# Kernel tuning notes

Measured on AMD Instinct MI355X. Metric: run time of the kernel, lower is better.

Reference implementation:

```python
import jax, jax.numpy as jnp
import numpy as np

DIM = 768
HID = 3072
HID2 = HID // 2
MAX_LEVEL = 8
N_LEV = MAX_LEVEL + 1
BATCH, SEQ = 2, 2048
EPS = 1e-5


def _layernorm(x, gamma, beta):
    m = jnp.mean(x, axis=-1, keepdims=True)
    v = jnp.mean(jnp.square(x - m), axis=-1, keepdims=True)
    return (x - m) * jax.lax.rsqrt(v + EPS) * gamma + beta


def setup_inputs() -> dict:
    key = jax.random.key(0)
    ks = jax.random.split(key, 12)
    s = 0.02
    return {
        "x": jax.random.normal(ks[0], (BATCH, SEQ, DIM), dtype=jnp.float32),
        "levels_info": jax.random.randint(ks[1], (SEQ, 4), 0, N_LEV, dtype=jnp.int32),
        "gamma": jnp.ones((DIM,), dtype=jnp.float32),
        "beta": jnp.zeros((DIM,), dtype=jnp.float32),
        "W1": jax.random.normal(ks[2], (DIM, HID), dtype=jnp.float32) * s,
        "b1": jnp.zeros((HID,), dtype=jnp.float32),
        "W2": jax.random.normal(ks[3], (HID, DIM), dtype=jnp.float32) * s,
        "b2": jnp.zeros((DIM,), dtype=jnp.float32),
        "A1": jax.random.normal(ks[4], (N_LEV, DIM, HID2), dtype=jnp.float32) * s,
        "a1b": jnp.zeros((N_LEV, HID2), dtype=jnp.float32),
        "A2": jax.random.normal(ks[5], (N_LEV, HID2, DIM), dtype=jnp.float32) * s,
        "a2b": jnp.zeros((N_LEV, DIM), dtype=jnp.float32),
        "lmw": jnp.ones((N_LEV,), dtype=jnp.float32)
        + jax.random.normal(ks[6], (N_LEV,), dtype=jnp.float32) * 0.1,
    }


def reference(x, levels_info, gamma, beta, W1, b1, W2, b2, A1, a1b, A2, a2b, lmw):
    # x: [B,S,D]
    x_norm = _layernorm(x, gamma, beta)
    # main MLP: Linear -> GELU (exact, torch default) -> Linear; dropout=0 is identity
    h = jax.nn.gelu(jnp.einsum("bsd,dh->bsh", x_norm, W1) + b1, approximate=False)
    main_out = jnp.einsum("bsh,hd->bsd", h, W2) + b2

    # per-token depth-indexed adapter routing
    depths = jnp.clip(levels_info[:, 0], 0, MAX_LEVEL)  # [S]
    level_adapted = jnp.zeros_like(main_out)
    for lvl in range(N_LEV):  # small fixed expert set
        mask = (depths == lvl).astype(x.dtype)[None, :, None]  # [1,S,1]
        hl = jax.nn.relu(jnp.einsum("bsd,dh->bsh", x_norm, A1[lvl]) + a1b[lvl])
        level_adapted = level_adapted + mask * (
            jnp.einsum("bsh,hd->bsd", hl, A2[lvl]) + a2b[lvl]
        )

    # softmax over the sequence axis (faithful to F.softmax(..., dim=0))
    mix = jax.nn.softmax(lmw[depths], axis=0)[None, :, None]  # [1,S,1]
    return main_out * (1.0 - mix) + level_adapted * mix
```

## Files before the change

### kernel.cpp

```cpp
#include <hip/hip_runtime.h>
#include <hip/hip_bf16.h>
#include <math.h>

typedef __bf16 bf16;
typedef __bf16 bf16x4 __attribute__((ext_vector_type(4)));
typedef __bf16 bf16x8 __attribute__((ext_vector_type(8)));
typedef float f32x4 __attribute__((ext_vector_type(4)));

#define DIM 768
#define HID 3072
#define HID2 1536
#define NLEV 9
#define SEQ 2048
#define ROWS 4096
#define MAXPAD 5248
#define MAXTILES 41

__device__ __forceinline__ void gld16(const void* g, void* l) {
    __builtin_amdgcn_global_load_lds(
        (const __attribute__((address_space(1))) void*)g,
        (__attribute__((address_space(3))) void*)l, 16, 0, 0);
}

__device__ __forceinline__ float fast_gelu(float v) {
    float v2 = v * v;
    float twou = v * (1.59576912f + 0.071354816f * v2);
    float t = __expf(twou);
    return v * t / (t + 1.0f);
}


__device__ __forceinline__ void ln_body(int row, float* sm,
                                        const float* __restrict__ x,
                                        const float* __restrict__ gamma,
                                        const float* __restrict__ beta,
                                        bf16* __restrict__ xn) {
    int tid = threadIdx.x;
    const float* xr = x + (size_t)row * DIM;
    float v0 = xr[tid], v1 = xr[tid + 256], v2 = xr[tid + 512];
    float s = v0 + v1 + v2;
    float q = v0 * v0 + v1 * v1 + v2 * v2;
    for (int off = 32; off; off >>= 1) {
        s += __shfl_down(s, off, 64);
        q += __shfl_down(q, off, 64);
    }
    int wv = tid >> 6, ln = tid & 63;
    if (ln == 0) { sm[wv] = s; sm[4 + wv] = q; }
    __syncthreads();
    if (tid == 0) {
        float S = sm[0] + sm[1] + sm[2] + sm[3];
        float Q = sm[4] + sm[5] + sm[6] + sm[7];
        float m = S * (1.0f / DIM);
        float var = Q * (1.0f / DIM) - m * m;
        sm[8] = m;
        sm[9] = rsqrtf(var + 1e-5f);
    }
    __syncthreads();
    float m = sm[8], r = sm[9];
    bf16* xo = xn + (size_t)row * DIM;
    xo[tid]       = (bf16)((v0 - m) * r * gamma[tid]       + beta[tid]);
    xo[tid + 256] = (bf16)((v1 - m) * r * gamma[tid + 256] + beta[tid + 256]);
    xo[tid + 512] = (bf16)((v2 - m) * r * gamma[tid + 512] + beta[tid + 512]);
}

__device__ __forceinline__ void transpose_body64(float* sm,
                                                 const float* __restrict__ inb,
                                                 bf16* __restrict__ outb,
                                                 int R, int C, int bx, int by) {
    int tid = threadIdx.x;
    int ty = tid >> 4;
    int tx4 = (tid & 15) * 4;
#pragma unroll
    for (int p = 0; p < 4; p++) {
        int rloc = p * 16 + ty;
        int row = by * 64 + rloc;
        float4 v = *(const float4*)(inb + (size_t)row * C + bx * 64 + tx4);
        sm[rloc * 65 + tx4 + 0] = v.x;
        sm[rloc * 65 + tx4 + 1] = v.y;
        sm[rloc * 65 + tx4 + 2] = v.z;
        sm[rloc * 65 + tx4 + 3] = v.w;
    }
    __syncthreads();
    int ch = tid & 7;
    int ocb = tid >> 3;
#pragma unroll
    for (int p = 0; p < 2; p++) {
        int oc = p * 32 + ocb;
        bf16x8 tmp;
#pragma unroll
        for (int k = 0; k < 8; k++) tmp[k] = (bf16)sm[(ch * 8 + k) * 65 + oc];
        *(bf16x8*)(outb + (size_t)(bx * 64 + oc) * R + by * 64 + ch * 8) = tmp;
    }
}

__device__ __forceinline__ void routing_body(float* sm,
                                             const int* __restrict__ levels_info,
                                             const float* __restrict__ lmw,
                                             float* __restrict__ mix,
                                             int* __restrict__ row_index,
                                             int* __restrict__ tile_meta,
                                             float* __restrict__ zbuf) {
    int* cnt = (int*)sm;
    int* cur = cnt + NLEV;
    int* off = cur + NLEV;
    float* mixv = (float*)(off + NLEV);
    int tid = threadIdx.x;
    if (tid < NLEV) { cnt[tid] = 0; cur[tid] = 0; }
    __syncthreads();
    for (int s = tid; s < SEQ; s += 256) {
        int d = levels_info[s * 4];
        d = d < 0 ? 0 : (d > 8 ? 8 : d);
        atomicAdd(&cnt[d], 1);
    }
    for (int i = tid; i < MAXPAD; i += 256) row_index[i] = -1;
    if (tid < 16) zbuf[tid] = 0.0f;
    __syncthreads();
    if (tid == 0) {
        float mx = lmw[0];
        for (int l = 1; l < NLEV; l++) mx = fmaxf(mx, lmw[l]);
        float denom = 0.f;
        for (int l = 0; l < NLEV; l++) denom += (float)cnt[l] * expf(lmw[l] - mx);
        float inv = 1.0f / denom;
        int running = 0, t = 0;
        for (int l = 0; l < NLEV; l++) {
            mixv[l] = expf(lmw[l] - mx) * inv;
            off[l] = running;
            int seg = (2 * cnt[l] + 127) & ~127;
            for (int k = 0; k < seg / 128; k++) tile_meta[t++] = l;
            running += seg;
        }
        for (; t < MAXTILES; t++) tile_meta[t] = -1;
    }
    __syncthreads();
    for (int s = tid; s < SEQ; s += 256) {
        int d = levels_info[s * 4];
        d = d < 0 ? 0 : (d > 8 ? 8 : d);
        int p = atomicAdd(&cur[d], 2);
        row_index[off[d] + p]     = s;
        row_index[off[d] + p + 1] = s + SEQ;
        mix[s] = mixv[d];
    }
}

__global__ __launch_bounds__(256) void prep_kernel(const float* __restrict__ x,
                                                   const int* __restrict__ levels_info,
                                                   const float* __restrict__ gamma,
                                                   const float* __restrict__ beta,
                                                   const float* __restrict__ W1,
                                                   const float* __restrict__ W2,
                                                   const float* __restrict__ A1,
                                                   const float* __restrict__ A2,
                                                   const float* __restrict__ lmw,
                                                   bf16* __restrict__ Xn,
                                                   bf16* __restrict__ W1t,
                                                   bf16* __restrict__ W2t,
                                                   bf16* __restrict__ A1t,
                                                   bf16* __restrict__ A2t,
                                                   float* __restrict__ mix,
                                                   int* __restrict__ row_index,
                                                   int* __restrict__ tile_meta,
                                                   float* __restrict__ zbuf) {
    __shared__ __align__(16) float sm[64 * 65];
    int bid = blockIdx.x;
    if (bid == 0) { routing_body(sm, levels_info, lmw, mix, row_index, tile_meta, zbuf); return; }
    bid -= 1;
    if (bid < ROWS) { ln_body(bid, sm, x, gamma, beta, Xn); return; }
    bid -= ROWS;
    if (bid < 576) {
        transpose_body64(sm, W1, W1t, DIM, HID, bid % 48, bid / 48);
        return;
    }
    bid -= 576;
    if (bid < 576) {
        transpose_body64(sm, W2, W2t, HID, DIM, bid % 12, bid / 12);
        return;
    }
    bid -= 576;
    if (bid < 2592) {
        int bz = bid / 288, r = bid % 288;
        transpose_body64(sm, A1 + (size_t)bz * DIM * HID2, A1t + (size_t)bz * DIM * HID2,
                         DIM, HID2, r % 24, r / 24);
        return;
    }
    bid -= 2592;
    {
        int bz = bid / 288, r = bid % 288;
        transpose_body64(sm, A2 + (size_t)bz * HID2 * DIM, A2t + (size_t)bz * HID2 * DIM,
                         HID2, DIM, r % 12, r / 12);
    }
}

__device__ __forceinline__ void gemm_loop_db(const bf16* ga0, const bf16* ga1,
                                             int stepa0, int stepa1,
                                             const bf16* gb0, const bf16* gb1, int stepb,
                                             bf16* As, bf16* Bs,
                                             f32x4 (&acc)[4][4], int ktiles) {
    int tid = threadIdx.x;
    int wv = tid >> 6;
    int lane = tid & 63;
    int wm = wv >> 1, wn = wv & 1;
    int swz = (lane >> 1) & 3;
    int achunk = ((lane >> 4) ^ swz) * 8;
    int aoff = ((wm * 64) + (lane & 15)) * 32 + achunk;
    int boff = ((wn * 64) + (lane & 15)) * 32 + achunk;
    gld16(ga0, As + wv * 512);
    gld16(ga1, As + 2048 + wv * 512);
    gld16(gb0, Bs + wv * 512);
    gld16(gb1, Bs + 2048 + wv * 512);
    ga0 += stepa0; ga1 += stepa1; gb0 += stepb; gb1 += stepb;
    for (int kt = 0; kt < ktiles; ++kt) {
        __syncthreads();
        int cur = (kt & 1) << 12;
        int nxt = cur ^ 4096;
        if (kt + 1 < ktiles) {
            gld16(ga0, As + nxt + wv * 512);
            gld16(ga1, As + nxt + 2048 + wv * 512);
            gld16(gb0, Bs + nxt + wv * 512);
            gld16(gb1, Bs + nxt + 2048 + wv * 512);
            ga0 += stepa0; ga1 += stepa1; gb0 += stepb; gb1 += stepb;
        }
        bf16x8 af[4], bfr[4];
#pragma unroll
        for (int i = 0; i < 4; i++) af[i] = *(const bf16x8*)(As + cur + aoff + i * 512);
#pragma unroll
        for (int j = 0; j < 4; j++) bfr[j] = *(const bf16x8*)(Bs + cur + boff + j * 512);
#pragma unroll
        for (int i = 0; i < 4; i++)
#pragma unroll
            for (int j = 0; j < 4; j++)
                acc[i][j] = __builtin_amdgcn_mfma_f32_16x16x32_bf16(af[i], bfr[j], acc[i][j], 0, 0, 0);
    }
}

#define ACC_INIT(acc) \
    _Pragma("unroll") for (int i = 0; i < 4; i++) \
    _Pragma("unroll") for (int j = 0; j < 4; j++) acc[i][j] = (f32x4){0.f, 0.f, 0.f, 0.f};

#define SWZ_CG(tid) (((tid) & 3) ^ (((tid) >> 3) & 3))

__global__ __launch_bounds__(256) void mlp1_kernel(const bf16* __restrict__ Xn,
                                                   const bf16* __restrict__ W1t,
                                                   const float* __restrict__ b1,
                                                   bf16* __restrict__ H,
                                                   const bf16* __restrict__ A1t,
                                                   const float* __restrict__ a1b,
                                                   const int* __restrict__ row_index,
                                                   const int* __restrict__ tile_meta,
                                                   const bf16* __restrict__ zbuf,
                                                   bf16* __restrict__ HL) {
    __shared__ __align__(16) bf16 As[8192], Bs[8192];
    int bid = blockIdx.x, tid = threadIdx.x;
    int r0 = tid >> 2, cg = SWZ_CG(tid);
    int lane = tid & 63, wv = tid >> 6, wm = wv >> 1, wn = wv & 1;
    f32x4 acc[4][4];
    ACC_INIT(acc);

    if (bid < 768) {
        int mb = (bid & 7) + 8 * ((bid >> 3) & 3);
        int nb = bid >> 5;
        const bf16* ga0 = Xn + (size_t)(mb * 128 + r0) * DIM + cg * 8;
        const bf16* ga1 = ga0 + (size_t)64 * DIM;
        const bf16* gb0 = W1t + (size_t)(nb * 128 + r0) * DIM + cg * 8;
        const bf16* gb1 = gb0 + (size_t)64 * DIM;
        gemm_loop_db(ga0, ga1, 32, 32, gb0, gb1, 32, As, Bs, acc, DIM / 32);
        int rbase = mb * 128 + wm * 64 + ((lane >> 4) << 2);
        int cbase = nb * 128 + wn * 64 + (lane & 15);
#pragma unroll
        for (int j = 0; j < 4; j++) {
            int c = cbase + j * 16;
            float bias = b1[c];
#pragma unroll
            for (int i = 0; i < 4; i++)
#pragma unroll
                for (int r = 0; r < 4; r++) {
                    int row = rbase + i * 16 + r;
                    float v = acc[i][j][r] + bias;
                    H[(size_t)row * HID + c] = (bf16)fast_gelu(v);
                }
        }
    } else {
        int t2 = bid - 768;
        int t = t2 % MAXTILES, nb = t2 / MAXTILES;
        int lvl = tile_meta[t];
        if (lvl < 0) return;
        int ridx0 = row_index[t * 128 + r0];
        int ridx1 = row_index[t * 128 + 64 + r0];
        const bf16* ga0 = (ridx0 >= 0) ? (Xn + (size_t)ridx0 * DIM + cg * 8) : zbuf;
        const bf16* ga1 = (ridx1 >= 0) ? (Xn + (size_t)ridx1 * DIM + cg * 8) : zbuf;
        int sa0 = (ridx0 >= 0) ? 32 : 0;
        int sa1 = (ridx1 >= 0) ? 32 : 0;
        const bf16* Bl = A1t + (size_t)lvl * HID2 * DIM;
        const bf16* gb0 = Bl + (size_t)(nb * 128 + r0) * DIM + cg * 8;
        const bf16* gb1 = gb0 + (size_t)64 * DIM;
        gemm_loop_db(ga0, ga1, sa0, sa1, gb0, gb1, 32, As, Bs, acc, DIM / 32);
        int rbase = wm * 64 + ((lane >> 4) << 2);
        int cbase = nb * 128 + wn * 64 + (lane & 15);
#pragma unroll
        for (int j = 0; j < 4; j++) {
            int c = cbase + j * 16;
            float bias = a1b[lvl * HID2 + c];
#pragma unroll
            for (int i = 0; i < 4; i++)
#pragma unroll
                for (int r = 0; r < 4; r++) {
                    int rl = rbase + i * 16 + r;
                    float v = acc[i][j][r] + bias;
                    HL[(size_t)(t * 128 + rl) * HID2 + c] = (bf16)fmaxf(v, 0.0f);
                }
        }
    }
}

__global__ __launch_bounds__(256) void mlp2_kernel(const bf16* __restrict__ H,
                                                   const bf16* __restrict__ W2t,
                                                   bf16* __restrict__ part,
                                                   const bf16* __restrict__ HL,
                                                   const bf16* __restrict__ A2t,
                                                   const float* __restrict__ a2b,
                                                   const int* __restrict__ row_index,
                                                   const int* __restrict__ tile_meta,
                                                   bf16* __restrict__ apart) {
    __shared__ __align__(16) bf16 As[8192], Bs[8192];
    int bid = blockIdx.x, tid = threadIdx.x;
    int r0 = tid >> 2, cg = SWZ_CG(tid);
    int lane = tid & 63, wv = tid >> 6, wm = wv >> 1, wn = wv & 1;
    f32x4 acc[4][4];
    ACC_INIT(acc);

    if (bid < 768) {
        int mb = (bid & 7) + 8 * ((bid >> 3) & 3);
        int rest = bid >> 5;
        int nb = rest % 6;
        int ks = rest / 6;
        const bf16* ga0 = H + (size_t)(mb * 128 + r0) * HID + ks * 768 + cg * 8;
        const bf16* ga1 = ga0 + (size_t)64 * HID;
        const bf16* gb0 = W2t + (size_t)(nb * 128 + r0) * HID + ks * 768 + cg * 8;
        const bf16* gb1 = gb0 + (size_t)64 * HID;
        gemm_loop_db(ga0, ga1, 32, 32, gb0, gb1, 32, As, Bs, acc, 24);
        bf16* pk = part + (size_t)ks * ROWS * DIM;
        int rbase = mb * 128 + wm * 64 + ((lane >> 4) << 2);
        int cbase = nb * 128 + wn * 64 + (lane & 15);
#pragma unroll
        for (int j = 0; j < 4; j++) {
            int c = cbase + j * 16;
#pragma unroll
            for (int i = 0; i < 4; i++)
#pragma unroll
                for (int r = 0; r < 4; r++) {
                    int row = rbase + i * 16 + r;
                    pk[(size_t)row * DIM + c] = (bf16)acc[i][j][r];
                }
        }
    } else {
        int t2 = bid - 768;
        int t = t2 % MAXTILES;
        int rest = t2 / MAXTILES;
        int nb = rest % 6;
        int ks = rest / 6;
        int lvl = tile_meta[t];
        if (lvl < 0) return;
        const bf16* ga0 = HL + (size_t)(t * 128 + r0) * HID2 + ks * 768 + cg * 8;
        const bf16* ga1 = ga0 + (size_t)64 * HID2;
        const bf16* Bl = A2t + (size_t)lvl * DIM * HID2;
        const bf16* gb0 = Bl + (size_t)(nb * 128 + r0) * HID2 + ks * 768 + cg * 8;
        const bf16* gb1 = gb0 + (size_t)64 * HID2;
        gemm_loop_db(ga0, ga1, 32, 32, gb0, gb1, 32, As, Bs, acc, 24);
        bf16* apk = apart + (size_t)ks * ROWS * DIM;
        int rbase = wm * 64 + ((lane >> 4) << 2);
        int cbase = nb * 128 + wn * 64 + (lane & 15);
#pragma unroll
        for (int i = 0; i < 4; i++)
#pragma unroll
            for (int r = 0; r < 4; r++) {
                int rl = rbase + i * 16 + r;
                int rg = row_index[t * 128 + rl];
                if (rg >= 0) {
#pragma unroll
                    for (int j = 0; j < 4; j++) {
                        int c = cbase + j * 16;
                        float v = acc[i][j][r] + (ks == 0 ? a2b[lvl * DIM + c] : 0.0f);
                        apk[(size_t)rg * DIM + c] = (bf16)v;
                    }
                }
            }
    }
}

__global__ __launch_bounds__(256) void combine_kernel(const bf16* __restrict__ part,
                                                      const bf16* __restrict__ apart,
                                                      const float* __restrict__ b2,
                                                      const float* __restrict__ mix,
                                                      float* __restrict__ out) {
    int i = blockIdx.x * 256 + threadIdx.x;
    int base = i * 4;
    int row = base / DIM;
    int c = base - row * DIM;
    float mx = mix[row & (SEQ - 1)];
    bf16x4 p0 = *(const bf16x4*)(part + base);
    bf16x4 p1 = *(const bf16x4*)(part + (size_t)1 * ROWS * DIM + base);
    bf16x4 p2 = *(const bf16x4*)(part + (size_t)2 * ROWS * DIM + base);
    bf16x4 p3 = *(const bf16x4*)(part + (size_t)3 * ROWS * DIM + base);
    bf16x4 a0 = *(const bf16x4*)(apart + base);
    bf16x4 a1 = *(const bf16x4*)(apart + (size_t)1 * ROWS * DIM + base);
    float4 o;
    float* po = &o.x;
#pragma unroll
    for (int k = 0; k < 4; k++) {
        float main_v = (float)p0[k] + (float)p1[k] + (float)p2[k] + (float)p3[k] + b2[c + k];
        float ap_v = (float)a0[k] + (float)a1[k];
        po[k] = (1.0f - mx) * main_v + mx * ap_v;
    }
    *(float4*)(out + base) = o;
}

extern "C" void kernel_launch(void* const* d_in, const int* in_sizes, int n_in,
                              void* d_out, int out_size, void* d_ws, size_t ws_size,
                              hipStream_t stream) {
    const float* x    = (const float*)d_in[0];
    const int* levels = (const int*)d_in[1];
    const float* gamma= (const float*)d_in[2];
    const float* beta = (const float*)d_in[3];
    const float* W1   = (const float*)d_in[4];
    const float* b1   = (const float*)d_in[5];
    const float* W2   = (const float*)d_in[6];
    const float* b2   = (const float*)d_in[7];
    const float* A1   = (const float*)d_in[8];
    const float* a1b  = (const float*)d_in[9];
    const float* A2   = (const float*)d_in[10];
    const float* a2b  = (const float*)d_in[11];
    const float* lmw  = (const float*)d_in[12];
    float* out = (float*)d_out;

    char* p = (char*)d_ws;
    auto alloc = [&](size_t bytes) {
        char* r = p;
        p += (bytes + 255) & ~(size_t)255;
        return r;
    };
    bf16* Xn   = (bf16*)alloc((size_t)ROWS * DIM * 2);
    bf16* W1t  = (bf16*)alloc((size_t)HID * DIM * 2);
    bf16* W2t  = (bf16*)alloc((size_t)DIM * HID * 2);
    bf16* A1t  = (bf16*)alloc((size_t)NLEV * HID2 * DIM * 2);
    bf16* A2t  = (bf16*)alloc((size_t)NLEV * DIM * HID2 * 2);
    bf16* H    = (bf16*)alloc((size_t)ROWS * HID * 2);
    bf16* HL   = (bf16*)alloc((size_t)MAXPAD * HID2 * 2);
    bf16* part = (bf16*)alloc((size_t)4 * ROWS * DIM * 2);
    bf16* apart= (bf16*)alloc((size_t)2 * ROWS * DIM * 2);
    float* mix = (float*)alloc(SEQ * 4);
    int* row_index = (int*)alloc(MAXPAD * 4);
    int* tile_meta = (int*)alloc(MAXTILES * 4);
    float* zbuf    = (float*)alloc(64);

    prep_kernel<<<dim3(1 + ROWS + 576 + 576 + 2592 + 2592), dim3(256), 0, stream>>>(
        x, levels, gamma, beta, W1, W2, A1, A2, lmw,
        Xn, W1t, W2t, A1t, A2t, mix, row_index, tile_meta, zbuf);

    mlp1_kernel<<<dim3(768 + MAXTILES * 12), dim3(256), 0, stream>>>(
        Xn, W1t, b1, H, A1t, a1b, row_index, tile_meta, (const bf16*)zbuf, HL);

    mlp2_kernel<<<dim3(768 + MAXTILES * 12), dim3(256), 0, stream>>>(
        H, W2t, part, HL, A2t, a2b, row_index, tile_meta, apart);

    combine_kernel<<<dim3(ROWS * DIM / 1024), dim3(256), 0, stream>>>(
        part, apart, b2, mix, out);
}
```

Measured before the change: 299.7 us.

## Replace LDS-staged GEMM loop with direct global-to-register MFMA operand loads

```diff
diff --git a/kernel.cpp b/kernel.cpp
--- a/kernel.cpp
+++ b/kernel.cpp
@@ -15,12 +15,6 @@
 #define ROWS 4096
 #define MAXPAD 5248
 #define MAXTILES 41
-
-__device__ __forceinline__ void gld16(const void* g, void* l) {
-    __builtin_amdgcn_global_load_lds(
-        (const __attribute__((address_space(1))) void*)g,
-        (__attribute__((address_space(3))) void*)l, 16, 0, 0);
-}
 
 __device__ __forceinline__ float fast_gelu(float v) {
     float v2 = v * v;
@@ -113,7 +107,7 @@
         atomicAdd(&cnt[d], 1);
     }
     for (int i = tid; i < MAXPAD; i += 256) row_index[i] = -1;
-    if (tid < 16) zbuf[tid] = 0.0f;
+    for (int i = tid; i < 512; i += 256) zbuf[i] = 0.0f;
     __syncthreads();
     if (tid == 0) {
         float mx = lmw[0];
@@ -190,53 +184,42 @@
     }
 }
 
-__device__ __forceinline__ void gemm_loop_db(const bf16* ga0, const bf16* ga1,
-                                             int stepa0, int stepa1,
-                                             const bf16* gb0, const bf16* gb1, int stepb,
-                                             bf16* As, bf16* Bs,
-                                             f32x4 (&acc)[4][4], int ktiles) {
-    int tid = threadIdx.x;
-    int wv = tid >> 6;
-    int lane = tid & 63;
-    int wm = wv >> 1, wn = wv & 1;
-    int swz = (lane >> 1) & 3;
-    int achunk = ((lane >> 4) ^ swz) * 8;
-    int aoff = ((wm * 64) + (lane & 15)) * 32 + achunk;
-    int boff = ((wn * 64) + (lane & 15)) * 32 + achunk;
-    gld16(ga0, As + wv * 512);
-    gld16(ga1, As + 2048 + wv * 512);
-    gld16(gb0, Bs + wv * 512);
-    gld16(gb1, Bs + 2048 + wv * 512);
-    ga0 += stepa0; ga1 += stepa1; gb0 += stepb; gb1 += stepb;
-    for (int kt = 0; kt < ktiles; ++kt) {
-        __syncthreads();
-        int cur = (kt & 1) << 12;
-        int nxt = cur ^ 4096;
-        if (kt + 1 < ktiles) {
-            gld16(ga0, As + nxt + wv * 512);
-            gld16(ga1, As + nxt + 2048 + wv * 512);
-            gld16(gb0, Bs + nxt + wv * 512);
-            gld16(gb1, Bs + nxt + 2048 + wv * 512);
-            ga0 += stepa0; ga1 += stepa1; gb0 += stepb; gb1 += stepb;
-        }
-        bf16x8 af[4], bfr[4];
-#pragma unroll
-        for (int i = 0; i < 4; i++) af[i] = *(const bf16x8*)(As + cur + aoff + i * 512);
-#pragma unroll
-        for (int j = 0; j < 4; j++) bfr[j] = *(const bf16x8*)(Bs + cur + boff + j * 512);
+__device__ __forceinline__ void gemm_k768(const bf16* pa0, const bf16* pa1,
+                                          const bf16* pa2, const bf16* pa3,
+                                          const bf16* pb0, const bf16* pb1,
+                                          const bf16* pb2, const bf16* pb3,
+                                          f32x4 (&acc)[4][4]) {
+    const bf16* pa[4] = {pa0, pa1, pa2, pa3};
+    const bf16* pb[4] = {pb0, pb1, pb2, pb3};
+    bf16x8 af[2][4], bfr[2][4];
+#pragma unroll
+    for (int i = 0; i < 4; i++) {
+        af[0][i]  = *(const bf16x8*)(pa[i]);
+        bfr[0][i] = *(const bf16x8*)(pb[i]);
+        af[1][i]  = *(const bf16x8*)(pa[i] + 32);
+        bfr[1][i] = *(const bf16x8*)(pb[i] + 32);
+    }
+#pragma unroll
+    for (int kt = 0; kt < 24; kt++) {
+        int s = kt & 1;
 #pragma unroll
         for (int i = 0; i < 4; i++)
 #pragma unroll
             for (int j = 0; j < 4; j++)
-                acc[i][j] = __builtin_amdgcn_mfma_f32_16x16x32_bf16(af[i], bfr[j], acc[i][j], 0, 0, 0);
+                acc[i][j] = __builtin_amdgcn_mfma_f32_16x16x32_bf16(af[s][i], bfr[s][j], acc[i][j], 0, 0, 0);
+        if (kt + 2 < 24) {
+#pragma unroll
+            for (int i = 0; i < 4; i++) {
+                af[s][i]  = *(const bf16x8*)(pa[i] + (kt + 2) * 32);
+                bfr[s][i] = *(const bf16x8*)(pb[i] + (kt + 2) * 32);
+            }
+        }
     }
 }
 
 #define ACC_INIT(acc) \
     _Pragma("unroll") for (int i = 0; i < 4; i++) \
     _Pragma("unroll") for (int j = 0; j < 4; j++) acc[i][j] = (f32x4){0.f, 0.f, 0.f, 0.f};
-
-#define SWZ_CG(tid) (((tid) & 3) ^ (((tid) >> 3) & 3))
 
 __global__ __launch_bounds__(256) void mlp1_kernel(const bf16* __restrict__ Xn,
                                                    const bf16* __restrict__ W1t,
@@ -248,23 +231,25 @@
                                                    const int* __restrict__ tile_meta,
                                                    const bf16* __restrict__ zbuf,
                                                    bf16* __restrict__ HL) {
-    __shared__ __align__(16) bf16 As[8192], Bs[8192];
     int bid = blockIdx.x, tid = threadIdx.x;
-    int r0 = tid >> 2, cg = SWZ_CG(tid);
     int lane = tid & 63, wv = tid >> 6, wm = wv >> 1, wn = wv & 1;
+    int lr = lane & 15, lc = (lane >> 4) * 8;
     f32x4 acc[4][4];
     ACC_INIT(acc);
 
     if (bid < 768) {
-        int mb = (bid & 7) + 8 * ((bid >> 3) & 3);
-        int nb = bid >> 5;
-        const bf16* ga0 = Xn + (size_t)(mb * 128 + r0) * DIM + cg * 8;
-        const bf16* ga1 = ga0 + (size_t)64 * DIM;
-        const bf16* gb0 = W1t + (size_t)(nb * 128 + r0) * DIM + cg * 8;
-        const bf16* gb1 = gb0 + (size_t)64 * DIM;
-        gemm_loop_db(ga0, ga1, 32, 32, gb0, gb1, 32, As, Bs, acc, DIM / 32);
+        int nb = (bid & 7) * 3 + ((bid >> 3) % 3);
+        int mb = bid / 24;
+        const bf16* pa[4];
+        const bf16* pb[4];
+#pragma unroll
+        for (int i = 0; i < 4; i++) {
+            pa[i] = Xn  + (size_t)(mb * 128 + wm * 64 + i * 16 + lr) * DIM + lc;
+            pb[i] = W1t + (size_t)(nb * 128 + wn * 64 + i * 16 + lr) * DIM + lc;
+        }
+        gemm_k768(pa[0], pa[1], pa[2], pa[3], pb[0], pb[1], pb[2], pb[3], acc);
         int rbase = mb * 128 + wm * 64 + ((lane >> 4) << 2);
-        int cbase = nb * 128 + wn * 64 + (lane & 15);
+        int cbase = nb * 128 + wn * 64 + lr;
 #pragma unroll
         for (int j = 0; j < 4; j++) {
             int c = cbase + j * 16;
@@ -274,27 +259,26 @@
 #pragma unroll
                 for (int r = 0; r < 4; r++) {
                     int row = rbase + i * 16 + r;
-                    float v = acc[i][j][r] + bias;
-                    H[(size_t)row * HID + c] = (bf16)fast_gelu(v);
+                    H[(size_t)row * HID + c] = (bf16)fast_gelu(acc[i][j][r] + bias);
                 }
         }
     } else {
         int t2 = bid - 768;
-        int t = t2 % MAXTILES, nb = t2 / MAXTILES;
+        int nb = t2 % 12, t = t2 / 12;
         int lvl = tile_meta[t];
         if (lvl < 0) return;
-        int ridx0 = row_index[t * 128 + r0];
-        int ridx1 = row_index[t * 128 + 64 + r0];
-        const bf16* ga0 = (ridx0 >= 0) ? (Xn + (size_t)ridx0 * DIM + cg * 8) : zbuf;
-        const bf16* ga1 = (ridx1 >= 0) ? (Xn + (size_t)ridx1 * DIM + cg * 8) : zbuf;
-        int sa0 = (ridx0 >= 0) ? 32 : 0;
-        int sa1 = (ridx1 >= 0) ? 32 : 0;
+        const bf16* pa[4];
+        const bf16* pb[4];
         const bf16* Bl = A1t + (size_t)lvl * HID2 * DIM;
-        const bf16* gb0 = Bl + (size_t)(nb * 128 + r0) * DIM + cg * 8;
-        const bf16* gb1 = gb0 + (size_t)64 * DIM;
-        gemm_loop_db(ga0, ga1, sa0, sa1, gb0, gb1, 32, As, Bs, acc, DIM / 32);
+#pragma unroll
+        for (int i = 0; i < 4; i++) {
+            int ridx = row_index[t * 128 + wm * 64 + i * 16 + lr];
+            pa[i] = (ridx >= 0) ? (Xn + (size_t)ridx * DIM + lc) : (zbuf + lc);
+            pb[i] = Bl + (size_t)(nb * 128 + wn * 64 + i * 16 + lr) * DIM + lc;
+        }
+        gemm_k768(pa[0], pa[1], pa[2], pa[3], pb[0], pb[1], pb[2], pb[3], acc);
         int rbase = wm * 64 + ((lane >> 4) << 2);
-        int cbase = nb * 128 + wn * 64 + (lane & 15);
+        int cbase = nb * 128 + wn * 64 + lr;
 #pragma unroll
         for (int j = 0; j < 4; j++) {
             int c = cbase + j * 16;
@@ -304,8 +288,7 @@
 #pragma unroll
                 for (int r = 0; r < 4; r++) {
                     int rl = rbase + i * 16 + r;
-                    float v = acc[i][j][r] + bias;
-                    HL[(size_t)(t * 128 + rl) * HID2 + c] = (bf16)fmaxf(v, 0.0f);
+                    HL[(size_t)(t * 128 + rl) * HID2 + c] = (bf16)fmaxf(acc[i][j][r] + bias, 0.0f);
                 }
         }
     }
@@ -320,26 +303,27 @@
                                                    const int* __restrict__ row_index,
                                                    const int* __restrict__ tile_meta,
                                                    bf16* __restrict__ apart) {
-    __shared__ __align__(16) bf16 As[8192], Bs[8192];
     int bid = blockIdx.x, tid = threadIdx.x;
-    int r0 = tid >> 2, cg = SWZ_CG(tid);
     int lane = tid & 63, wv = tid >> 6, wm = wv >> 1, wn = wv & 1;
+    int lr = lane & 15, lc = (lane >> 4) * 8;
     f32x4 acc[4][4];
     ACC_INIT(acc);
 
     if (bid < 768) {
-        int mb = (bid & 7) + 8 * ((bid >> 3) & 3);
-        int rest = bid >> 5;
-        int nb = rest % 6;
-        int ks = rest / 6;
-        const bf16* ga0 = H + (size_t)(mb * 128 + r0) * HID + ks * 768 + cg * 8;
-        const bf16* ga1 = ga0 + (size_t)64 * HID;
-        const bf16* gb0 = W2t + (size_t)(nb * 128 + r0) * HID + ks * 768 + cg * 8;
-        const bf16* gb1 = gb0 + (size_t)64 * HID;
-        gemm_loop_db(ga0, ga1, 32, 32, gb0, gb1, 32, As, Bs, acc, 24);
+        int c24 = (bid & 7) * 3 + ((bid >> 3) % 3);
+        int nb = c24 >> 2, ks = c24 & 3;
+        int mb = bid / 24;
+        const bf16* pa[4];
+        const bf16* pb[4];
+#pragma unroll
+        for (int i = 0; i < 4; i++) {
+            pa[i] = H   + (size_t)(mb * 128 + wm * 64 + i * 16 + lr) * HID + ks * 768 + lc;
+            pb[i] = W2t + (size_t)(nb * 128 + wn * 64 + i * 16 + lr) * HID + ks * 768 + lc;
+        }
+        gemm_k768(pa[0], pa[1], pa[2], pa[3], pb[0], pb[1], pb[2], pb[3], acc);
         bf16* pk = part + (size_t)ks * ROWS * DIM;
         int rbase = mb * 128 + wm * 64 + ((lane >> 4) << 2);
-        int cbase = nb * 128 + wn * 64 + (lane & 15);
+        int cbase = nb * 128 + wn * 64 + lr;
 #pragma unroll
         for (int j = 0; j < 4; j++) {
             int c = cbase + j * 16;
@@ -353,21 +337,23 @@
         }
     } else {
         int t2 = bid - 768;
-        int t = t2 % MAXTILES;
-        int rest = t2 / MAXTILES;
-        int nb = rest % 6;
-        int ks = rest / 6;
+        int cc = t2 % 12;
+        int nb = cc >> 1, ks = cc & 1;
+        int t = t2 / 12;
         int lvl = tile_meta[t];
         if (lvl < 0) return;
-        const bf16* ga0 = HL + (size_t)(t * 128 + r0) * HID2 + ks * 768 + cg * 8;
-        const bf16* ga1 = ga0 + (size_t)64 * HID2;
+        const bf16* pa[4];
+        const bf16* pb[4];
         const bf16* Bl = A2t + (size_t)lvl * DIM * HID2;
-        const bf16* gb0 = Bl + (size_t)(nb * 128 + r0) * HID2 + ks * 768 + cg * 8;
-        const bf16* gb1 = gb0 + (size_t)64 * HID2;
-        gemm_loop_db(ga0, ga1, 32, 32, gb0, gb1, 32, As, Bs, acc, 24);
+#pragma unroll
+        for (int i = 0; i < 4; i++) {
+            pa[i] = HL + (size_t)(t * 128 + wm * 64 + i * 16 + lr) * HID2 + ks * 768 + lc;
+            pb[i] = Bl + (size_t)(nb * 128 + wn * 64 + i * 16 + lr) * HID2 + ks * 768 + lc;
+        }
+        gemm_k768(pa[0], pa[1], pa[2], pa[3], pb[0], pb[1], pb[2], pb[3], acc);
         bf16* apk = apart + (size_t)ks * ROWS * DIM;
         int rbase = wm * 64 + ((lane >> 4) << 2);
-        int cbase = nb * 128 + wn * 64 + (lane & 15);
+        int cbase = nb * 128 + wn * 64 + lr;
 #pragma unroll
         for (int i = 0; i < 4; i++)
 #pragma unroll
@@ -449,7 +435,7 @@
     float* mix = (float*)alloc(SEQ * 4);
     int* row_index = (int*)alloc(MAXPAD * 4);
     int* tile_meta = (int*)alloc(MAXTILES * 4);
-    float* zbuf    = (float*)alloc(64);
+    float* zbuf    = (float*)alloc(2048);
 
     prep_kernel<<<dim3(1 + ROWS + 576 + 576 + 2592 + 2592), dim3(256), 0, stream>>>(
         x, levels, gamma, beta, W1, W2, A1, A2, lmw,
```

Measured after the change: 409.1 us. +36.5%, slower.
